# Kernel optimization log

Hardware: AMD Instinct MI355X
Metric: run time of the kernel (lower is better)

Reference implementation:

```python
import jax, jax.numpy as jnp
import numpy as np

B, N1, N2, D, H = 32, 331, 256, 256, 8  # batch, gene tokens (=num_pathway), path tokens (=dim), dim, heads
DH = D // H


def setup_inputs() -> dict:
    key = jax.random.key(0)
    ks = jax.random.split(key, 20)
    s = 0.05

    def rn(k, shape):
        return jax.random.normal(k, shape, dtype=jnp.float32) * s

    return {
        "x1": jax.random.normal(ks[0], (B, N1, D), dtype=jnp.float32),
        "x2": jax.random.normal(ks[1], (B, N2, D), dtype=jnp.float32),
        # routing network: Linear(2D->D), LayerNorm(D), GELU, Linear(D->4)
        "r_w1": rn(ks[2], (D, 2 * D)), "r_b1": jnp.zeros((D,), jnp.float32),
        "r_g": jnp.ones((D,), jnp.float32), "r_beta": jnp.zeros((D,), jnp.float32),
        "r_w2": rn(ks[3], (4, D)), "r_b2": jnp.zeros((4,), jnp.float32),
        # LinearFusion: Linear(D->D) + ELU
        "lin_w": rn(ks[4], (D, D)), "lin_b": jnp.zeros((D,), jnp.float32),
        # AddFusion (n1>n2 branch): linear2 = Linear(D->D)+ELU, linear3 = Linear(D->num_pathway)+ELU
        "add_w2": rn(ks[5], (D, D)), "add_b2": jnp.zeros((D,), jnp.float32),
        "add_w3": rn(ks[6], (N1, D)), "add_b3": jnp.zeros((N1,), jnp.float32),
        # AttentionFusion: MultiheadAttention(D, 8 heads) packed in-proj + out-proj
        "attn_win": rn(ks[7], (3 * D, D)), "attn_bin": jnp.zeros((3 * D,), jnp.float32),
        "attn_wout": rn(ks[8], (D, D)), "attn_bout": jnp.zeros((D,), jnp.float32),
    }


def _moe_forward(x1, x2, r_w1, r_b1, r_g, r_beta, r_w2, r_b2,
                 lin_w, lin_b, add_w2, add_b2, add_w3, add_b3,
                 attn_win, attn_bin, attn_wout, attn_bout):
    # ---- routing network (soft mode) ----
    m = jnp.concatenate([x1.mean(axis=1), x2.mean(axis=1)], axis=-1)  # [B, 2D]
    h = m @ r_w1.T + r_b1
    mu = h.mean(axis=-1, keepdims=True)
    var = ((h - mu) ** 2).mean(axis=-1, keepdims=True)
    h = (h - mu) / jnp.sqrt(var + 1e-5) * r_g + r_beta
    h = jax.nn.gelu(h, approximate=False)
    logits = h @ r_w2.T + r_b2                                        # [B, 4]
    w = jax.nn.softmax(logits, axis=-1)

    # ---- expert 0: LinearFusion ----
    comb = jnp.concatenate([x1, x2], axis=1)                          # [B, N1+N2, D]
    lo = jax.nn.elu(comb @ lin_w.T + lin_b)
    g0, i0 = lo[:, :N1, :], lo[:, N1:, :]

    # ---- expert 1: AddFusion (n1 > n2 branch; requires N2 == D) ----
    x1l = jax.nn.elu(x1 @ add_w2.T + add_b2)                          # [B, N1, D]
    # linear3 on x2.permute(0,2,1): [B, D, N2] @ W3^T -> [B, D, N1], permute back
    x2l = jax.nn.elu(jnp.einsum('bnd,pn->bpd', x2, add_w3) + add_b3[None, :, None])
    x_out = x1l + x2l                                                 # [B, N1, D]
    g1, i1 = x_out, x_out[:, :N2, :]

    # ---- expert 2: AttentionFusion (8-head MHA over concatenated tokens) ----
    qkv = comb @ attn_win.T + attn_bin                                # [B, S, 3D]
    q, k, v = jnp.split(qkv, 3, axis=-1)
    S = N1 + N2

    def heads(t):
        return t.reshape(B, S, H, DH)

    q, k, v = heads(q), heads(k), heads(v)
    scores = jnp.einsum('bqhd,bkhd->bhqk', q, k) / jnp.sqrt(jnp.float32(DH))
    attn = jax.nn.softmax(scores, axis=-1)
    o = jnp.einsum('bhqk,bkhd->bqhd', attn, v).reshape(B, S, D)
    o = o @ attn_wout.T + attn_bout
    g2, i2 = o[:, :N1, :], o[:, N1:, :]

    # ---- expert 3: IdentityFusion ----
    g3, i3 = x1, x2

    # ---- soft weighted combination over experts ----
    gene = jnp.einsum('be,ebnd->bnd', w, jnp.stack([g0, g1, g2, g3]))
    img = jnp.einsum('be,ebnd->bnd', w, jnp.stack([i0, i1, i2, i3]))
    return gene, img


def reference(x1, x2, r_w1, r_b1, r_g, r_beta, r_w2, r_b2,
              lin_w, lin_b, add_w2, add_b2, add_w3, add_b3,
              attn_win, attn_bin, attn_wout, attn_bout):
    return _moe_forward(x1, x2, r_w1, r_b1, r_g, r_beta, r_w2, r_b2,
                        lin_w, lin_b, add_w2, add_b2, add_w3, add_b3,
                        attn_win, attn_bin, attn_wout, attn_bout)
```

## Files before the change

### kernel.cpp

```cpp
#include <hip/hip_runtime.h>
#include <hip/hip_bf16.h>
#include <math.h>

#define Bb 32
#define N1c 331
#define N2c 256
#define Dc 256
#define Hc 8
#define DHc 32
#define Sc 587

__device__ __forceinline__ float eluf(float x) { return x > 0.f ? x : expm1f(x); }

__device__ __forceinline__ unsigned int packbf2(float x, float y) {
  unsigned int bx = __float_as_uint(x);
  unsigned int by = __float_as_uint(y);
  bx = (bx + 0x8000u) >> 16;
  by = (by + 0x8000u) & 0xffff0000u;
  return bx | by;
}

__device__ __forceinline__ float block_reduce_sum(float v, float* red) {
#pragma unroll
  for (int off = 32; off > 0; off >>= 1) v += __shfl_down(v, off, 64);
  const int lane = threadIdx.x & 63, wid = threadIdx.x >> 6;
  __syncthreads();
  if (lane == 0) red[wid] = v;
  __syncthreads();
  return red[0] + red[1] + red[2] + red[3];
}

__global__ __launch_bounds__(256) void routing_kernel(
    const float* __restrict__ x1, const float* __restrict__ x2,
    const float* __restrict__ r_w1, const float* __restrict__ r_b1,
    const float* __restrict__ r_g, const float* __restrict__ r_beta,
    const float* __restrict__ r_w2, const float* __restrict__ r_b2,
    float* __restrict__ wout) {
  const int b = blockIdx.x, t = threadIdx.x;
  __shared__ float m[512];
  __shared__ float red[4];

  float s = 0.f;
  const float* xp = x1 + (size_t)b * N1c * Dc + t;
  for (int n = 0; n < N1c; ++n) s += xp[(size_t)n * Dc];
  m[t] = s * (1.f / N1c);
  s = 0.f;
  const float* xp2 = x2 + (size_t)b * N2c * Dc + t;
  for (int n = 0; n < N2c; ++n) s += xp2[(size_t)n * Dc];
  m[256 + t] = s * (1.f / N2c);
  __syncthreads();

  float hv = r_b1[t];
  const float* wr = r_w1 + (size_t)t * 512;
#pragma unroll 4
  for (int k = 0; k < 512; k += 4) {
    float4 wv = *(const float4*)(wr + k);
    hv = fmaf(wv.x, m[k], hv);
    hv = fmaf(wv.y, m[k + 1], hv);
    hv = fmaf(wv.z, m[k + 2], hv);
    hv = fmaf(wv.w, m[k + 3], hv);
  }
  float mu = block_reduce_sum(hv, red) * (1.f / 256.f);
  float dv = hv - mu;
  float var = block_reduce_sum(dv * dv, red) * (1.f / 256.f);
  float hn = dv * rsqrtf(var + 1e-5f) * r_g[t] + r_beta[t];
  float ge = 0.5f * hn * (1.f + erff(hn * 0.70710678118654752f));

  float l0 = block_reduce_sum(ge * r_w2[0 * 256 + t], red) + r_b2[0];
  float l1 = block_reduce_sum(ge * r_w2[1 * 256 + t], red) + r_b2[1];
  float l2 = block_reduce_sum(ge * r_w2[2 * 256 + t], red) + r_b2[2];
  float l3 = block_reduce_sum(ge * r_w2[3 * 256 + t], red) + r_b2[3];
  if (t == 0) {
    float mx = fmaxf(fmaxf(l0, l1), fmaxf(l2, l3));
    float e0 = __expf(l0 - mx), e1 = __expf(l1 - mx), e2 = __expf(l2 - mx), e3 = __expf(l3 - mx);
    float inv = 1.f / (e0 + e1 + e2 + e3);
    wout[b * 4 + 0] = e0 * inv;
    wout[b * 4 + 1] = e1 * inv;
    wout[b * 4 + 2] = e2 * inv;
    wout[b * 4 + 3] = e3 * inv;
  }
}

template <int ACT, int AMODE>
__global__ __launch_bounds__(256) void gemm_xwT(
    const float* __restrict__ A, const float* __restrict__ x1,
    const float* __restrict__ x2, const float* __restrict__ W,
    const float* __restrict__ bias, float* __restrict__ C, int ldc, int M,
    int N, int K) {
  __shared__ float As[16][68];
  __shared__ float Bs[16][68];
  const int tid = threadIdx.x;
  const int m0 = blockIdx.y * 64;
  const int n0 = blockIdx.x * 64;
  const int tx = tid & 15, ty = tid >> 4;
  float acc[4][4] = {};

  const int sa_m = tid >> 2;
  const int sa_k = (tid & 3) * 4;

  int grow = m0 + sa_m;
  const bool rowok = grow < M;
  int crow = rowok ? grow : (M - 1);
  const float* arow;
  if (AMODE == 0) {
    arow = A + (size_t)crow * K;
  } else {
    int bidx = crow / Sc;
    int sidx = crow - bidx * Sc;
    arow = (sidx < N1c) ? (x1 + ((size_t)bidx * N1c + sidx) * Dc)
                        : (x2 + ((size_t)bidx * N2c + (sidx - N1c)) * Dc);
  }
  const float* wrow = W + (size_t)(n0 + sa_m) * K;

  for (int k0 = 0; k0 < K; k0 += 16) {
    float4 av = rowok ? *(const float4*)(arow + k0 + sa_k)
                      : make_float4(0.f, 0.f, 0.f, 0.f);
    float4 wv = *(const float4*)(wrow + k0 + sa_k);
    __syncthreads();
    As[sa_k + 0][sa_m] = av.x;
    As[sa_k + 1][sa_m] = av.y;
    As[sa_k + 2][sa_m] = av.z;
    As[sa_k + 3][sa_m] = av.w;
    Bs[sa_k + 0][sa_m] = wv.x;
    Bs[sa_k + 1][sa_m] = wv.y;
    Bs[sa_k + 2][sa_m] = wv.z;
    Bs[sa_k + 3][sa_m] = wv.w;
    __syncthreads();
#pragma unroll
    for (int kk = 0; kk < 16; ++kk) {
      float4 a = *(const float4*)&As[kk][ty * 4];
      float4 bv = *(const float4*)&Bs[kk][tx * 4];
      acc[0][0] = fmaf(a.x, bv.x, acc[0][0]);
      acc[0][1] = fmaf(a.x, bv.y, acc[0][1]);
      acc[0][2] = fmaf(a.x, bv.z, acc[0][2]);
      acc[0][3] = fmaf(a.x, bv.w, acc[0][3]);
      acc[1][0] = fmaf(a.y, bv.x, acc[1][0]);
      acc[1][1] = fmaf(a.y, bv.y, acc[1][1]);
      acc[1][2] = fmaf(a.y, bv.z, acc[1][2]);
      acc[1][3] = fmaf(a.y, bv.w, acc[1][3]);
      acc[2][0] = fmaf(a.z, bv.x, acc[2][0]);
      acc[2][1] = fmaf(a.z, bv.y, acc[2][1]);
      acc[2][2] = fmaf(a.z, bv.z, acc[2][2]);
      acc[2][3] = fmaf(a.z, bv.w, acc[2][3]);
      acc[3][0] = fmaf(a.w, bv.x, acc[3][0]);
      acc[3][1] = fmaf(a.w, bv.y, acc[3][1]);
      acc[3][2] = fmaf(a.w, bv.z, acc[3][2]);
      acc[3][3] = fmaf(a.w, bv.w, acc[3][3]);
    }
  }
  const int col = n0 + tx * 4;
  float4 bv4 = *(const float4*)(bias + col);
#pragma unroll
  for (int i = 0; i < 4; ++i) {
    int row = m0 + ty * 4 + i;
    if (row >= M) continue;
    float4 r;
    r.x = acc[i][0] + bv4.x;
    r.y = acc[i][1] + bv4.y;
    r.z = acc[i][2] + bv4.z;
    r.w = acc[i][3] + bv4.w;
    if (ACT == 1) {
      r.x = eluf(r.x);
      r.y = eluf(r.y);
      r.z = eluf(r.z);
      r.w = eluf(r.w);
    }
    *(float4*)(C + (size_t)row * ldc + col) = r;
  }
}

__global__ __launch_bounds__(256) void gemm_w3x2(
    const float* __restrict__ w3, const float* __restrict__ x2,
    const float* __restrict__ b3, float* __restrict__ xout) {
  const int bz = blockIdx.z;
  const int p0 = blockIdx.y * 64;
  const int d0 = blockIdx.x * 64;
  __shared__ float As[16][68];
  __shared__ float Bs[16][68];
  const int tid = threadIdx.x;
  const int tx = tid & 15, ty = tid >> 4;
  float acc[4][4] = {};

  const int sa_m = tid >> 2;
  const int sa_k = (tid & 3) * 4;
  const int sb_k = tid >> 4;
  const int sb_d = (tid & 15) * 4;

  const float* x2b = x2 + (size_t)bz * N2c * Dc;
  int prow = p0 + sa_m;
  const bool rowok = prow < N1c;
  const float* arow = w3 + (size_t)(rowok ? prow : (N1c - 1)) * N2c;

  for (int k0 = 0; k0 < N2c; k0 += 16) {
    float4 av = rowok ? *(const float4*)(arow + k0 + sa_k)
                      : make_float4(0.f, 0.f, 0.f, 0.f);
    float4 bv = *(const float4*)(x2b + (size_t)(k0 + sb_k) * Dc + d0 + sb_d);
    __syncthreads();
    As[sa_k + 0][sa_m] = av.x;
    As[sa_k + 1][sa_m] = av.y;
    As[sa_k + 2][sa_m] = av.z;
    As[sa_k + 3][sa_m] = av.w;
    Bs[sb_k][sb_d + 0] = bv.x;
    Bs[sb_k][sb_d + 1] = bv.y;
    Bs[sb_k][sb_d + 2] = bv.z;
    Bs[sb_k][sb_d + 3] = bv.w;
    __syncthreads();
#pragma unroll
    for (int kk = 0; kk < 16; ++kk) {
      float4 a = *(const float4*)&As[kk][ty * 4];
      float4 bb = *(const float4*)&Bs[kk][tx * 4];
      acc[0][0] = fmaf(a.x, bb.x, acc[0][0]);
      acc[0][1] = fmaf(a.x, bb.y, acc[0][1]);
      acc[0][2] = fmaf(a.x, bb.z, acc[0][2]);
      acc[0][3] = fmaf(a.x, bb.w, acc[0][3]);
      acc[1][0] = fmaf(a.y, bb.x, acc[1][0]);
      acc[1][1] = fmaf(a.y, bb.y, acc[1][1]);
      acc[1][2] = fmaf(a.y, bb.z, acc[1][2]);
      acc[1][3] = fmaf(a.y, bb.w, acc[1][3]);
      acc[2][0] = fmaf(a.z, bb.x, acc[2][0]);
      acc[2][1] = fmaf(a.z, bb.y, acc[2][1]);
      acc[2][2] = fmaf(a.z, bb.z, acc[2][2]);
      acc[2][3] = fmaf(a.z, bb.w, acc[2][3]);
      acc[3][0] = fmaf(a.w, bb.x, acc[3][0]);
      acc[3][1] = fmaf(a.w, bb.y, acc[3][1]);
      acc[3][2] = fmaf(a.w, bb.z, acc[3][2]);
      acc[3][3] = fmaf(a.w, bb.w, acc[3][3]);
    }
  }
#pragma unroll
  for (int i = 0; i < 4; ++i) {
    int p = p0 + ty * 4 + i;
    if (p >= N1c) continue;
    float bbias = b3[p];
    float* cp = xout + ((size_t)bz * N1c + p) * Dc + d0 + tx * 4;
    float4 cur = *(float4*)cp;
    cur.x += eluf(acc[i][0] + bbias);
    cur.y += eluf(acc[i][1] + bbias);
    cur.z += eluf(acc[i][2] + bbias);
    cur.w += eluf(acc[i][3] + bbias);
    *(float4*)cp = cur;
  }
}

__global__ __launch_bounds__(256, 2) void attn_kernel(
    const float* __restrict__ qkv, float* __restrict__ o_pre) {
  const int bh = blockIdx.x;
  const int chunk = blockIdx.y;
  const int b = bh >> 3, h = bh & 7;
  const int tid = threadIdx.x;
  __shared__ unsigned int Kl[Sc * 16];
  __shared__ unsigned int Vl[Sc * 16];
  const size_t base = (size_t)b * Sc * 768;

  for (int p = tid; p < Sc * 16; p += 256) {
    int s = p >> 4, dp = (p & 15) * 2;
    const float* kr = qkv + base + (size_t)s * 768 + 256 + h * 32 + dp;
    float2 k2 = *(const float2*)kr;
    float2 v2 = *(const float2*)(kr + 256);
    Kl[p] = packbf2(k2.x, k2.y);
    Vl[p] = packbf2(v2.x, v2.y);
  }
  __syncthreads();

  const int qstart = chunk ? 296 : 0;
  const int qcnt = chunk ? 291 : 296;
  const int r0 = qstart + tid;
  const int r1 = qstart + 256 + tid;
  const bool has1 = (256 + tid) < qcnt;

  const float scale = 0.17677669529663688f;
  float q0[32], q1[32], acc0[32] = {}, acc1[32] = {};
  {
    const float* qp = qkv + base + (size_t)r0 * 768 + h * 32;
#pragma unroll
    for (int i = 0; i < 32; i += 4) {
      float4 v = *(const float4*)(qp + i);
      q0[i] = v.x * scale;
      q0[i + 1] = v.y * scale;
      q0[i + 2] = v.z * scale;
      q0[i + 3] = v.w * scale;
    }
    if (has1) {
      const float* qp1 = qkv + base + (size_t)r1 * 768 + h * 32;
#pragma unroll
      for (int i = 0; i < 32; i += 4) {
        float4 v = *(const float4*)(qp1 + i);
        q1[i] = v.x * scale;
        q1[i + 1] = v.y * scale;
        q1[i + 2] = v.z * scale;
        q1[i + 3] = v.w * scale;
      }
    } else {
#pragma unroll
      for (int i = 0; i < 32; ++i) q1[i] = 0.f;
    }
  }
  float m0r = -1e30f, l0 = 0.f, m1r = -1e30f, l1 = 0.f;

  for (int j = 0; j < Sc; ++j) {
    float kf[32];
    {
      const uint4* kp = reinterpret_cast<const uint4*>(Kl + (j << 4));
#pragma unroll
      for (int qq = 0; qq < 4; ++qq) {
        uint4 u = kp[qq];
        kf[qq * 8 + 0] = __uint_as_float(u.x << 16);
        kf[qq * 8 + 1] = __uint_as_float(u.x & 0xffff0000u);
        kf[qq * 8 + 2] = __uint_as_float(u.y << 16);
        kf[qq * 8 + 3] = __uint_as_float(u.y & 0xffff0000u);
        kf[qq * 8 + 4] = __uint_as_float(u.z << 16);
        kf[qq * 8 + 5] = __uint_as_float(u.z & 0xffff0000u);
        kf[qq * 8 + 6] = __uint_as_float(u.w << 16);
        kf[qq * 8 + 7] = __uint_as_float(u.w & 0xffff0000u);
      }
    }
    float s0 = 0.f, s1 = 0.f;
#pragma unroll
    for (int i = 0; i < 32; ++i) {
      s0 = fmaf(q0[i], kf[i], s0);
      s1 = fmaf(q1[i], kf[i], s1);
    }
    if (s0 > m0r) {
      float c = __expf(m0r - s0);
      l0 *= c;
#pragma unroll
      for (int i = 0; i < 32; ++i) acc0[i] *= c;
      m0r = s0;
    }
    float p0 = __expf(s0 - m0r);
    l0 += p0;
    if (s1 > m1r) {
      float c = __expf(m1r - s1);
      l1 *= c;
#pragma unroll
      for (int i = 0; i < 32; ++i) acc1[i] *= c;
      m1r = s1;
    }
    float p1 = __expf(s1 - m1r);
    l1 += p1;

    float vf[32];
    {
      const uint4* vp = reinterpret_cast<const uint4*>(Vl + (j << 4));
#pragma unroll
      for (int qq = 0; qq < 4; ++qq) {
        uint4 u = vp[qq];
        vf[qq * 8 + 0] = __uint_as_float(u.x << 16);
        vf[qq * 8 + 1] = __uint_as_float(u.x & 0xffff0000u);
        vf[qq * 8 + 2] = __uint_as_float(u.y << 16);
        vf[qq * 8 + 3] = __uint_as_float(u.y & 0xffff0000u);
        vf[qq * 8 + 4] = __uint_as_float(u.z << 16);
        vf[qq * 8 + 5] = __uint_as_float(u.z & 0xffff0000u);
        vf[qq * 8 + 6] = __uint_as_float(u.w << 16);
        vf[qq * 8 + 7] = __uint_as_float(u.w & 0xffff0000u);
      }
    }
#pragma unroll
    for (int i = 0; i < 32; ++i) {
      acc0[i] = fmaf(p0, vf[i], acc0[i]);
      acc1[i] = fmaf(p1, vf[i], acc1[i]);
    }
  }

  {
    float inv0 = 1.f / l0;
    float* op = o_pre + ((size_t)b * Sc + r0) * 256 + h * 32;
#pragma unroll
    for (int i = 0; i < 32; i += 4) {
      float4 v;
      v.x = acc0[i] * inv0;
      v.y = acc0[i + 1] * inv0;
      v.z = acc0[i + 2] * inv0;
      v.w = acc0[i + 3] * inv0;
      *(float4*)(op + i) = v;
    }
    if (has1) {
      float inv1 = 1.f / l1;
      float* op1 = o_pre + ((size_t)b * Sc + r1) * 256 + h * 32;
#pragma unroll
      for (int i = 0; i < 32; i += 4) {
        float4 v;
        v.x = acc1[i] * inv1;
        v.y = acc1[i + 1] * inv1;
        v.z = acc1[i + 2] * inv1;
        v.w = acc1[i + 3] * inv1;
        *(float4*)(op1 + i) = v;
      }
    }
  }
}

__global__ __launch_bounds__(256) void combine_kernel(
    const float* __restrict__ lo, const float* __restrict__ xout,
    const float* __restrict__ o, const float* __restrict__ x1,
    const float* __restrict__ x2, const float* __restrict__ wb,
    float* __restrict__ out) {
  const int gene4 = Bb * N1c * Dc / 4;
  const int img4 = Bb * N2c * Dc / 4;
  int idx = blockIdx.x * 256 + threadIdx.x;
  if (idx >= gene4 + img4) return;
  if (idx < gene4) {
    int e = idx * 4;
    int b = e / (N1c * Dc);
    int rem = e - b * (N1c * Dc);
    int n = rem >> 8, d = rem & 255;
    float w0 = wb[b * 4 + 0], w1 = wb[b * 4 + 1], w2 = wb[b * 4 + 2],
          w3 = wb[b * 4 + 3];
    float4 g0 = *(const float4*)(lo + ((size_t)b * Sc + n) * Dc + d);
    float4 g1 = *(const float4*)(xout + ((size_t)b * N1c + n) * Dc + d);
    float4 g2 = *(const float4*)(o + ((size_t)b * Sc + n) * Dc + d);
    float4 g3 = *(const float4*)(x1 + e);
    float4 r;
    r.x = w0 * g0.x + w1 * g1.x + w2 * g2.x + w3 * g3.x;
    r.y = w0 * g0.y + w1 * g1.y + w2 * g2.y + w3 * g3.y;
    r.z = w0 * g0.z + w1 * g1.z + w2 * g2.z + w3 * g3.z;
    r.w = w0 * g0.w + w1 * g1.w + w2 * g2.w + w3 * g3.w;
    *(float4*)(out + e) = r;
  } else {
    int e = (idx - gene4) * 4;
    int b = e >> 16;
    int rem = e & 65535;
    int n = rem >> 8, d = rem & 255;
    float w0 = wb[b * 4 + 0], w1 = wb[b * 4 + 1], w2 = wb[b * 4 + 2],
          w3 = wb[b * 4 + 3];
    float4 g0 = *(const float4*)(lo + ((size_t)b * Sc + N1c + n) * Dc + d);
    float4 g1 = *(const float4*)(xout + ((size_t)b * N1c + n) * Dc + d);
    float4 g2 = *(const float4*)(o + ((size_t)b * Sc + N1c + n) * Dc + d);
    float4 g3 = *(const float4*)(x2 + e);
    float4 r;
    r.x = w0 * g0.x + w1 * g1.x + w2 * g2.x + w3 * g3.x;
    r.y = w0 * g0.y + w1 * g1.y + w2 * g2.y + w3 * g3.y;
    r.z = w0 * g0.z + w1 * g1.z + w2 * g2.z + w3 * g3.z;
    r.w = w0 * g0.w + w1 * g1.w + w2 * g2.w + w3 * g3.w;
    *(float4*)(out + (size_t)(Bb * N1c * Dc) + e) = r;
  }
}

extern "C" void kernel_launch(void* const* d_in, const int* in_sizes, int n_in,
                              void* d_out, int out_size, void* d_ws,
                              size_t ws_size, hipStream_t stream) {
  const float* x1 = (const float*)d_in[0];
  const float* x2 = (const float*)d_in[1];
  const float* r_w1 = (const float*)d_in[2];
  const float* r_b1 = (const float*)d_in[3];
  const float* r_g = (const float*)d_in[4];
  const float* r_beta = (const float*)d_in[5];
  const float* r_w2 = (const float*)d_in[6];
  const float* r_b2 = (const float*)d_in[7];
  const float* lin_w = (const float*)d_in[8];
  const float* lin_b = (const float*)d_in[9];
  const float* add_w2 = (const float*)d_in[10];
  const float* add_b2 = (const float*)d_in[11];
  const float* add_w3 = (const float*)d_in[12];
  const float* add_b3 = (const float*)d_in[13];
  const float* attn_win = (const float*)d_in[14];
  const float* attn_bin = (const float*)d_in[15];
  const float* attn_wout = (const float*)d_in[16];
  const float* attn_bout = (const float*)d_in[17];
  float* out = (float*)d_out;
  float* ws = (float*)d_ws;

  float* lo = ws;
  float* xout = ws + 4808704;
  float* qkvb = ws + 7520256;
  float* o_pre = ws + 21946368;
  float* wroute = ws + 26755072;
  float* ob = qkvb;

  const int MS = Bb * Sc;
  const int M1 = Bb * N1c;

  routing_kernel<<<Bb, 256, 0, stream>>>(x1, x2, r_w1, r_b1, r_g, r_beta, r_w2,
                                         r_b2, wroute);
  gemm_xwT<1, 1><<<dim3(4, (MS + 63) / 64), 256, 0, stream>>>(
      nullptr, x1, x2, lin_w, lin_b, lo, Dc, MS, Dc, Dc);
  gemm_xwT<1, 0><<<dim3(4, (M1 + 63) / 64), 256, 0, stream>>>(
      x1, nullptr, nullptr, add_w2, add_b2, xout, Dc, M1, Dc, Dc);
  gemm_w3x2<<<dim3(4, 6, Bb), 256, 0, stream>>>(add_w3, x2, add_b3, xout);
  gemm_xwT<0, 1><<<dim3(12, (MS + 63) / 64), 256, 0, stream>>>(
      nullptr, x1, x2, attn_win, attn_bin, qkvb, 768, MS, 768, Dc);
  attn_kernel<<<dim3(Bb * Hc, 2), 256, 0, stream>>>(qkvb, o_pre);
  gemm_xwT<0, 0><<<dim3(4, (MS + 63) / 64), 256, 0, stream>>>(
      o_pre, nullptr, nullptr, attn_wout, attn_bout, ob, Dc, MS, Dc, Dc);
  combine_kernel<<<4696, 256, 0, stream>>>(lo, xout, ob, x1, x2, wroute, out);
}
```

Before: 801.9 us.

## Run LinearFusion GEMM on bf16 MFMA with packed bf16 inputs

Replaces the fp32 FMA tiled GEMM for the LinearFusion expert with a bf16 MFMA kernel (16x16x32). New pack kernels convert the concatenated x1/x2 activations and lin_w to bf16 in workspace first. The A tile goes through swizzled LDS, and W fragments are read directly from global memory. This cuts the ALU cost of one of the larger GEMMs. In exchange it adds two extra kernel launches plus bf16 conversion traffic, and lowers the precision of that expert's output.

After: 817.1 us. About the same (+1.9%).

```diff
diff --git a/kernel.cpp b/kernel.cpp
--- a/kernel.cpp
+++ b/kernel.cpp
@@ -10,6 +10,10 @@
 #define DHc 32
 #define Sc 587
 
+typedef short bfrag __attribute__((ext_vector_type(8)));
+typedef float f32x4 __attribute__((ext_vector_type(4)));
+typedef unsigned short u16x8 __attribute__((ext_vector_type(8)));
+
 __device__ __forceinline__ float eluf(float x) { return x > 0.f ? x : expm1f(x); }
 
 __device__ __forceinline__ unsigned int packbf2(float x, float y) {
@@ -18,6 +22,15 @@
   bx = (bx + 0x8000u) >> 16;
   by = (by + 0x8000u) & 0xffff0000u;
   return bx | by;
+}
+
+__device__ __forceinline__ unsigned short f2bf(float f) {
+  unsigned int u = __float_as_uint(f);
+  return (unsigned short)((u + 0x7fffu + ((u >> 16) & 1u)) >> 16);
+}
+
+__device__ __forceinline__ f32x4 mfma16(bfrag a, bfrag b, f32x4 c) {
+  return __builtin_amdgcn_mfma_f32_16x16x32_bf16(a, b, c, 0, 0, 0);
 }
 
 __device__ __forceinline__ float block_reduce_sum(float v, float* red) {
@@ -239,6 +252,102 @@
     cur.z += eluf(acc[i][2] + bbias);
     cur.w += eluf(acc[i][3] + bbias);
     *(float4*)cp = cur;
+  }
+}
+
+__global__ __launch_bounds__(256) void pack_comb(const float* __restrict__ x1,
+                                                 const float* __restrict__ x2,
+                                                 __hip_bfloat16* __restrict__ combB) {
+  int flat8 = (blockIdx.x * 256 + threadIdx.x) * 8;
+  int b = flat8 / 150272;
+  int rem = flat8 - b * 150272;
+  int s = rem >> 8, d = rem & 255;
+  const float* src = (s < N1c) ? (x1 + ((size_t)b * N1c + s) * Dc + d)
+                               : (x2 + ((size_t)b * N2c + (s - N1c)) * Dc + d);
+  float4 v0 = *(const float4*)(src);
+  float4 v1 = *(const float4*)(src + 4);
+  u16x8 o;
+  o[0] = f2bf(v0.x); o[1] = f2bf(v0.y); o[2] = f2bf(v0.z); o[3] = f2bf(v0.w);
+  o[4] = f2bf(v1.x); o[5] = f2bf(v1.y); o[6] = f2bf(v1.z); o[7] = f2bf(v1.w);
+  *(u16x8*)((unsigned short*)combB + flat8) = o;
+}
+
+__global__ __launch_bounds__(256) void pack_wlin(const float* __restrict__ lin_w,
+                                                 __hip_bfloat16* __restrict__ wB) {
+  int e = (blockIdx.x * 256 + threadIdx.x) * 8;
+  float4 v0 = *(const float4*)(lin_w + e);
+  float4 v1 = *(const float4*)(lin_w + e + 4);
+  u16x8 o;
+  o[0] = f2bf(v0.x); o[1] = f2bf(v0.y); o[2] = f2bf(v0.z); o[3] = f2bf(v0.w);
+  o[4] = f2bf(v1.x); o[5] = f2bf(v1.y); o[6] = f2bf(v1.z); o[7] = f2bf(v1.w);
+  *(u16x8*)((unsigned short*)wB + e) = o;
+}
+
+__global__ __launch_bounds__(256) void gemm_lo_mfma(
+    const __hip_bfloat16* __restrict__ A, const __hip_bfloat16* __restrict__ W,
+    const float* __restrict__ bias, float* __restrict__ C) {
+  const int M = 18784, K = 256;
+  const int tid = threadIdx.x, lane = tid & 63, wid = tid >> 6;
+  const int wr = wid >> 1, wc = wid & 1;
+  const int m0 = blockIdx.y * 128, n0 = blockIdx.x * 64;
+  __shared__ __align__(16) __hip_bfloat16 As[4096];
+
+  const __hip_bfloat16* src[2];
+#pragma unroll
+  for (int i = 0; i < 2; ++i) {
+    int o = i * 256 + tid;
+    int row = o >> 2, sl = o & 3;
+    int g = sl ^ ((row >> 1) & 3);
+    int ar = m0 + row;
+    if (ar >= M) ar = M - 1;
+    src[i] = A + (size_t)ar * K + g * 8;
+  }
+  __hip_bfloat16* dst0 = As + (size_t)tid * 8;
+  __hip_bfloat16* dst1 = As + (size_t)(256 + tid) * 8;
+
+  const __hip_bfloat16* wrow0 =
+      W + (size_t)(n0 + wc * 32 + (lane & 15)) * K + (lane >> 4) * 8;
+  const __hip_bfloat16* wrow1 = wrow0 + (size_t)16 * K;
+
+  f32x4 acc[4][2];
+#pragma unroll
+  for (int i = 0; i < 4; ++i)
+#pragma unroll
+    for (int j = 0; j < 2; ++j) acc[i][j] = (f32x4){0.f, 0.f, 0.f, 0.f};
+
+#pragma unroll 1
+  for (int ks = 0; ks < 8; ++ks) {
+    bfrag av0 = *(const bfrag*)(src[0] + ks * 32);
+    bfrag av1 = *(const bfrag*)(src[1] + ks * 32);
+    bfrag wf0 = *(const bfrag*)(wrow0 + ks * 32);
+    bfrag wf1 = *(const bfrag*)(wrow1 + ks * 32);
+    __syncthreads();
+    *(bfrag*)dst0 = av0;
+    *(bfrag*)dst1 = av1;
+    __syncthreads();
+#pragma unroll
+    for (int mf = 0; mf < 4; ++mf) {
+      int r = wr * 64 + mf * 16 + (lane & 15);
+      bfrag af = *(const bfrag*)(As + r * 32 + (((lane >> 4) ^ ((r >> 1) & 3)) * 8));
+      acc[mf][0] = mfma16(af, wf0, acc[mf][0]);
+      acc[mf][1] = mfma16(af, wf1, acc[mf][1]);
+    }
+  }
+
+#pragma unroll
+  for (int nf = 0; nf < 2; ++nf) {
+    int col = n0 + wc * 32 + nf * 16 + (lane & 15);
+    float bc = bias[col];
+#pragma unroll
+    for (int mf = 0; mf < 4; ++mf) {
+      int rbase = m0 + wr * 64 + mf * 16 + (lane >> 4) * 4;
+#pragma unroll
+      for (int reg = 0; reg < 4; ++reg) {
+        int r = rbase + reg;
+        if (r >= M) continue;
+        C[(size_t)r * 256 + col] = eluf(acc[mf][nf][reg] + bc);
+      }
+    }
   }
 }
 
@@ -467,13 +576,17 @@
   float* wroute = ws + 26755072;
   float* ob = qkvb;
 
+  __hip_bfloat16* combB = (__hip_bfloat16*)(ws + 7520256);
+  __hip_bfloat16* wBlin = (__hip_bfloat16*)((char*)(ws + 7520256) + 9617408);
+
   const int MS = Bb * Sc;
   const int M1 = Bb * N1c;
 
   routing_kernel<<<Bb, 256, 0, stream>>>(x1, x2, r_w1, r_b1, r_g, r_beta, r_w2,
                                          r_b2, wroute);
-  gemm_xwT<1, 1><<<dim3(4, (MS + 63) / 64), 256, 0, stream>>>(
-      nullptr, x1, x2, lin_w, lin_b, lo, Dc, MS, Dc, Dc);
+  pack_comb<<<2348, 256, 0, stream>>>(x1, x2, combB);
+  pack_wlin<<<32, 256, 0, stream>>>(lin_w, wBlin);
+  gemm_lo_mfma<<<dim3(4, 147), 256, 0, stream>>>(combB, wBlin, lin_b, lo);
   gemm_xwT<1, 0><<<dim3(4, (M1 + 63) / 64), 256, 0, stream>>>(
       x1, nullptr, nullptr, add_w2, add_b2, xout, Dc, M1, Dc, Dc);
   gemm_w3x2<<<dim3(4, 6, Bb), 256, 0, stream>>>(add_w3, x2, add_b3, xout);
```
